# Optimization experiments

Measured on AMD Instinct MI355X. Metric: run time of the kernel, lower is better.

## Reference

```python
import jax, jax.numpy as jnp
import numpy as np

NUM_EXPERTS = 8
HIDDEN = 1024
INTER = 1024
TOKENS = 2048
TOPK = 2


def setup_inputs() -> dict:
    key = jax.random.key(0)
    ks = jax.random.split(key, 7)
    hidden_states = jax.random.normal(ks[0], (TOKENS, HIDDEN), dtype=jnp.float32)
    router_weights = jax.random.uniform(ks[1], (TOKENS, TOPK), dtype=jnp.float32)
    selected_experts = jax.random.randint(ks[2], (TOKENS, TOPK), 0, NUM_EXPERTS, dtype=jnp.int32)
    token_per_expert = jax.random.randint(ks[3], (NUM_EXPERTS,), 0, 512, dtype=jnp.int32)
    # torch Linear weight layout is [out, in]; chunked along out-dim into E experts.
    # gate/up: [E, INTER, HIDDEN]; down: [E, HIDDEN, INTER]
    scale_h = 1.0 / np.sqrt(HIDDEN)
    scale_i = 1.0 / np.sqrt(INTER)
    gate_w = jax.random.normal(ks[4], (NUM_EXPERTS, INTER, HIDDEN), dtype=jnp.float32) * scale_h
    up_w = jax.random.normal(ks[5], (NUM_EXPERTS, INTER, HIDDEN), dtype=jnp.float32) * scale_h
    down_w = jax.random.normal(ks[6], (NUM_EXPERTS, HIDDEN, INTER), dtype=jnp.float32) * scale_i
    return {
        "hidden_states": hidden_states,
        "router_weights": router_weights,
        "selected_experts": selected_experts,
        "token_per_expert": token_per_expert,
        "gate_w": gate_w,
        "up_w": up_w,
        "down_w": down_w,
    }


def reference(hidden_states, router_weights, selected_experts, token_per_expert, gate_w, up_w, down_w):
    # Math equivalent of permute -> grouped GEMM (gate/up SwiGLU, down) -> unpermute+weighted combine.
    # Each (token, k) pair is routed to expert selected_experts[t,k] and scaled by router_weights[t,k]
    # (cast to fp32 as in the original), then summed over k.
    # Grouped GEMM out = x @ W_e^T; we evaluate every expert densely over all tokens and
    # combine with a one-hot routing matrix (clean, fully vectorized reference).
    x = hidden_states  # [T, H]
    g = jnp.einsum('th,eih->eti', x, gate_w)          # [E, T, I]
    u = jnp.einsum('th,eih->eti', x, up_w)            # [E, T, I]
    h = jax.nn.silu(g) * u                            # [E, T, I]
    out_e = jnp.einsum('eti,ehi->eth', h, down_w)     # [E, T, H]
    # combine[t, e] = sum_k router_weights[t, k] * 1[selected_experts[t, k] == e]
    onehot = jax.nn.one_hot(selected_experts, NUM_EXPERTS, dtype=jnp.float32)  # [T, K, E]
    combine = jnp.einsum('tk,tke->te', router_weights.astype(jnp.float32), onehot)  # [T, E]
    y = jnp.einsum('te,eth->th', combine, out_e)      # [T, H]
    return y
```

## Files before the change

kernel.cpp:

```cpp
#include <hip/hip_runtime.h>

#define HID   1024
#define NEXP  8
#define NPAIR 4096
#define BMPAD 128
#define PERM_MAX (NPAIR + NEXP * BMPAD)
#define MT_MAX (PERM_MAX / 128)

typedef unsigned short u16;
typedef __attribute__((ext_vector_type(8))) short bf16x8;
typedef __attribute__((ext_vector_type(4))) float f32x4;
typedef __attribute__((ext_vector_type(4))) unsigned short us4;

static __device__ __forceinline__ u16 f2bf(float f) {
  union { float f; unsigned u; } v; v.f = f;
  unsigned u = v.u;
  unsigned r = (u + 0x7fffu + ((u >> 16) & 1u)) >> 16;
  return (u16)r;
}

static __device__ __forceinline__ void gload16(const void* g, void* l) {
  __builtin_amdgcn_global_load_lds(
      (const __attribute__((address_space(1))) unsigned int*)g,
      (__attribute__((address_space(3))) unsigned int*)l, 16, 0, 0);
}

static __device__ __forceinline__ f32x4 mfma_bf16(bf16x8 a, bf16x8 b, f32x4 c) {
  return __builtin_amdgcn_mfma_f32_16x16x32_bf16(a, b, c, 0, 0, 0);
}

__global__ __launch_bounds__(256) void k_prep(const float* __restrict__ x,
                                              u16* __restrict__ xb,
                                              float* __restrict__ out) {
  int i = blockIdx.x * 256 + threadIdx.x;
  int base = i * 8;
  f32x4 v0 = *(const f32x4*)(x + base);
  f32x4 v1 = *(const f32x4*)(x + base + 4);
  us4 a = { f2bf(v0[0]), f2bf(v0[1]), f2bf(v0[2]), f2bf(v0[3]) };
  us4 b = { f2bf(v1[0]), f2bf(v1[1]), f2bf(v1[2]), f2bf(v1[3]) };
  *(us4*)(xb + base)     = a;
  *(us4*)(xb + base + 4) = b;
  f32x4 z = {0.f, 0.f, 0.f, 0.f};
  *(f32x4*)(out + base)     = z;
  *(f32x4*)(out + base + 4) = z;
}

__global__ __launch_bounds__(256) void k_convw(const float* __restrict__ g,
                                               const float* __restrict__ u,
                                               const float* __restrict__ d,
                                               u16* __restrict__ gb,
                                               u16* __restrict__ ub,
                                               u16* __restrict__ db) {
  const long NTH = 3L << 20;
  for (long i = (long)blockIdx.x * 256 + threadIdx.x; i < NTH; i += (long)gridDim.x * 256) {
    int which = (int)(i >> 20);
    long off = (i & ((1L << 20) - 1)) * 8;
    const float* src = which == 0 ? g : (which == 1 ? u : d);
    u16* dst = which == 0 ? gb : (which == 1 ? ub : db);
    f32x4 v0 = *(const f32x4*)(src + off);
    f32x4 v1 = *(const f32x4*)(src + off + 4);
    us4 a = { f2bf(v0[0]), f2bf(v0[1]), f2bf(v0[2]), f2bf(v0[3]) };
    us4 b = { f2bf(v1[0]), f2bf(v1[1]), f2bf(v1[2]), f2bf(v1[3]) };
    *(us4*)(dst + off)     = a;
    *(us4*)(dst + off + 4) = b;
  }
}

__global__ __launch_bounds__(256) void k_route(const int* __restrict__ sel,
                                               int* __restrict__ hdr,
                                               int* __restrict__ perm) {
  __shared__ int cnt[NEXP];
  __shared__ int cur[NEXP];
  int tid = threadIdx.x;
  if (tid < NEXP) cnt[tid] = 0;
  __syncthreads();
  for (int p = tid; p < NPAIR; p += 256) atomicAdd(&cnt[sel[p]], 1);
  __syncthreads();
  if (tid == 0) {
    int acc = 0;
    for (int e = 0; e < NEXP; e++) {
      hdr[e] = acc;
      cur[e] = acc;
      acc += (cnt[e] + 127) & ~127;
    }
    hdr[NEXP] = acc;
  }
  __syncthreads();
  for (int i = tid; i < PERM_MAX; i += 256) perm[i] = -1;
  __syncthreads();
  for (int p = tid; p < NPAIR; p += 256) {
    int e = sel[p];
    int slot = atomicAdd(&cur[e], 1);
    perm[slot] = p;
  }
}

__global__ __launch_bounds__(256) void k_gateup(const u16* __restrict__ xb,
                                                const u16* __restrict__ gwb,
                                                const u16* __restrict__ uwb,
                                                const int* __restrict__ hdr,
                                                const int* __restrict__ perm,
                                                u16* __restrict__ hbuf) {
  __shared__ __align__(16) u16 lA[128 * 64];
  __shared__ __align__(16) u16 lBg[64 * 64];
  __shared__ __align__(16) u16 lBu[64 * 64];

  const int tid = threadIdx.x, lane = tid & 63, wv = tid >> 6;
  const int n0 = blockIdx.x * 64, m0 = blockIdx.y * 128;
  const int total = hdr[NEXP];
  if (m0 >= total) return;
  int e = 0;
  #pragma unroll
  for (int k = 1; k < NEXP; k++) if (m0 >= hdr[k]) e = k;

  const u16* srcA[4]; u16* dstA[4];
  #pragma unroll
  for (int j = 0; j < 4; j++) {
    int rt = wv * 32 + j * 8 + (lane >> 3);
    int p = perm[m0 + rt];
    int tok = (p < 0) ? 0 : (p >> 1);
    int sw = (lane & 7) ^ (rt & 7);
    srcA[j] = xb + (size_t)tok * HID + sw * 8;
    dstA[j] = &lA[(wv * 32 + j * 8) * 64];
  }
  const u16* srcG[2]; const u16* srcU[2]; int dstBo[2];
  const size_t eb = (size_t)e * (1 << 20);
  #pragma unroll
  for (int j = 0; j < 2; j++) {
    int rt = wv * 16 + j * 8 + (lane >> 3);
    int sw = (lane & 7) ^ (rt & 7);
    srcG[j] = gwb + eb + (size_t)(n0 + rt) * HID + sw * 8;
    srcU[j] = uwb + eb + (size_t)(n0 + rt) * HID + sw * 8;
    dstBo[j] = (wv * 16 + j * 8) * 64;
  }

  const int wm = wv >> 1, wn = wv & 1;
  const int fr = lane & 15, fq = lane >> 4;

  f32x4 accg[4][2], accu[4][2];
  #pragma unroll
  for (int a = 0; a < 4; a++)
    #pragma unroll
    for (int b = 0; b < 2; b++) {
      accg[a][b] = (f32x4){0.f, 0.f, 0.f, 0.f};
      accu[a][b] = (f32x4){0.f, 0.f, 0.f, 0.f};
    }

  for (int kk = 0; kk < HID / 64; kk++) {
    const int k0 = kk * 64;
    #pragma unroll
    for (int j = 0; j < 4; j++) gload16(srcA[j] + k0, dstA[j]);
    #pragma unroll
    for (int j = 0; j < 2; j++) {
      gload16(srcG[j] + k0, &lBg[dstBo[j]]);
      gload16(srcU[j] + k0, &lBu[dstBo[j]]);
    }
    __syncthreads();
    #pragma unroll
    for (int kk2 = 0; kk2 < 2; kk2++) {
      bf16x8 af[4], bg[2], bu[2];
      #pragma unroll
      for (int m2 = 0; m2 < 4; m2++) {
        int r = wm * 64 + m2 * 16 + fr, q = kk2 * 4 + fq;
        af[m2] = *(const bf16x8*)&lA[r * 64 + (q ^ (r & 7)) * 8];
      }
      #pragma unroll
      for (int n2 = 0; n2 < 2; n2++) {
        int r = wn * 32 + n2 * 16 + fr, q = kk2 * 4 + fq;
        bg[n2] = *(const bf16x8*)&lBg[r * 64 + (q ^ (r & 7)) * 8];
        bu[n2] = *(const bf16x8*)&lBu[r * 64 + (q ^ (r & 7)) * 8];
      }
      #pragma unroll
      for (int m2 = 0; m2 < 4; m2++)
        #pragma unroll
        for (int n2 = 0; n2 < 2; n2++) {
          accg[m2][n2] = mfma_bf16(af[m2], bg[n2], accg[m2][n2]);
          accu[m2][n2] = mfma_bf16(af[m2], bu[n2], accu[m2][n2]);
        }
    }
    __syncthreads();
  }

  #pragma unroll
  for (int m2 = 0; m2 < 4; m2++)
    #pragma unroll
    for (int n2 = 0; n2 < 2; n2++)
      #pragma unroll
      for (int q = 0; q < 4; q++) {
        int row = m0 + wm * 64 + m2 * 16 + fq * 4 + q;
        int col = n0 + wn * 32 + n2 * 16 + fr;
        float g = accg[m2][n2][q];
        float u = accu[m2][n2][q];
        float h = (g / (1.0f + __expf(-g))) * u;
        hbuf[(size_t)row * HID + col] = f2bf(h);
      }
}

__global__ __launch_bounds__(256) void k_down(const u16* __restrict__ hbuf,
                                              const u16* __restrict__ dwb,
                                              const int* __restrict__ hdr,
                                              const int* __restrict__ perm,
                                              const float* __restrict__ rw,
                                              float* __restrict__ out) {
  __shared__ __align__(16) u16 lA[128 * 64];
  __shared__ __align__(16) u16 lB[64 * 64];

  const int tid = threadIdx.x, lane = tid & 63, wv = tid >> 6;
  const int n0 = blockIdx.x * 64, m0 = blockIdx.y * 128;
  const int total = hdr[NEXP];
  if (m0 >= total) return;
  int e = 0;
  #pragma unroll
  for (int k = 1; k < NEXP; k++) if (m0 >= hdr[k]) e = k;

  const u16* srcA[4]; u16* dstA[4];
  #pragma unroll
  for (int j = 0; j < 4; j++) {
    int rt = wv * 32 + j * 8 + (lane >> 3);
    int sw = (lane & 7) ^ (rt & 7);
    srcA[j] = hbuf + (size_t)(m0 + rt) * HID + sw * 8;
    dstA[j] = &lA[(wv * 32 + j * 8) * 64];
  }
  const u16* srcB[2]; int dstBo[2];
  const size_t eb = (size_t)e * (1 << 20);
  #pragma unroll
  for (int j = 0; j < 2; j++) {
    int rt = wv * 16 + j * 8 + (lane >> 3);
    int sw = (lane & 7) ^ (rt & 7);
    srcB[j] = dwb + eb + (size_t)(n0 + rt) * HID + sw * 8;
    dstBo[j] = (wv * 16 + j * 8) * 64;
  }

  const int wm = wv >> 1, wn = wv & 1;
  const int fr = lane & 15, fq = lane >> 4;

  f32x4 acc[4][2];
  #pragma unroll
  for (int a = 0; a < 4; a++)
    #pragma unroll
    for (int b = 0; b < 2; b++) acc[a][b] = (f32x4){0.f, 0.f, 0.f, 0.f};

  for (int kk = 0; kk < HID / 64; kk++) {
    const int k0 = kk * 64;
    #pragma unroll
    for (int j = 0; j < 4; j++) gload16(srcA[j] + k0, dstA[j]);
    #pragma unroll
    for (int j = 0; j < 2; j++) gload16(srcB[j] + k0, &lB[dstBo[j]]);
    __syncthreads();
    #pragma unroll
    for (int kk2 = 0; kk2 < 2; kk2++) {
      bf16x8 af[4], bf[2];
      #pragma unroll
      for (int m2 = 0; m2 < 4; m2++) {
        int r = wm * 64 + m2 * 16 + fr, q = kk2 * 4 + fq;
        af[m2] = *(const bf16x8*)&lA[r * 64 + (q ^ (r & 7)) * 8];
      }
      #pragma unroll
      for (int n2 = 0; n2 < 2; n2++) {
        int r = wn * 32 + n2 * 16 + fr, q = kk2 * 4 + fq;
        bf[n2] = *(const bf16x8*)&lB[r * 64 + (q ^ (r & 7)) * 8];
      }
      #pragma unroll
      for (int m2 = 0; m2 < 4; m2++)
        #pragma unroll
        for (int n2 = 0; n2 < 2; n2++)
          acc[m2][n2] = mfma_bf16(af[m2], bf[n2], acc[m2][n2]);
    }
    __syncthreads();
  }

  #pragma unroll
  for (int m2 = 0; m2 < 4; m2++)
    #pragma unroll
    for (int q = 0; q < 4; q++) {
      int row = m0 + wm * 64 + m2 * 16 + fq * 4 + q;
      int p = perm[row];
      if (p < 0) continue;
      int t = p >> 1;
      float w = rw[p];
      #pragma unroll
      for (int n2 = 0; n2 < 2; n2++) {
        int col = n0 + wn * 32 + n2 * 16 + fr;
        atomicAdd(&out[(size_t)t * HID + col], acc[m2][n2][q] * w);
      }
    }
}

extern "C" void kernel_launch(void* const* d_in, const int* in_sizes, int n_in,
                              void* d_out, int out_size, void* d_ws, size_t ws_size,
                              hipStream_t stream) {
  const float* x   = (const float*)d_in[0];
  const float* rw  = (const float*)d_in[1];
  const int*   sel = (const int*)d_in[2];
  const float* gw  = (const float*)d_in[4];
  const float* uw  = (const float*)d_in[5];
  const float* dw  = (const float*)d_in[6];
  float* out = (float*)d_out;

  char* ws = (char*)d_ws;
  int*  hdr  = (int*)ws;
  int*  perm = (int*)(ws + 1024);
  u16*  xb   = (u16*)(ws + (1 << 16));
  u16*  gwb  = xb + (2 << 20);
  u16*  uwb  = gwb + (8 << 20);
  u16*  dwb  = uwb + (8 << 20);
  u16*  hbuf = dwb + (8 << 20);

  k_prep <<<dim3(1024), dim3(256), 0, stream>>>(x, xb, out);
  k_convw<<<dim3(4096), dim3(256), 0, stream>>>(gw, uw, dw, gwb, uwb, dwb);
  k_route<<<dim3(1),    dim3(256), 0, stream>>>(sel, hdr, perm);
  k_gateup<<<dim3(16, MT_MAX), dim3(256), 0, stream>>>(xb, gwb, uwb, hdr, perm, hbuf);
  k_down  <<<dim3(16, MT_MAX), dim3(256), 0, stream>>>(hbuf, dwb, hdr, perm, rw, out);
}
```

Before: 114.4 us.

## Pre-permute activations and remap GEMM grids to expert-major tile loops

Weight conversion and output zeroing are merged into one fixed-grid kernel, and activations are gathered and converted into a permuted bf16 buffer by a new kernel. The GEMM kernels no longer do an indirect per-row gather. Both GEMM kernels now use a 1D grid indexed by expert, N tile and M-tile slot, with each block looping over that expert's M tiles at a stride of 8. This drops the blocks that exited early and keeps the same expert's weights hot across consecutive tiles. The cost is an extra pass writing and reading the permuted activation buffer, and possible imbalance when one expert has many more M tiles than others.

Result: slower. 133.9 us (+17.1%).

```diff
diff --git a/kernel.cpp b/kernel.cpp
--- a/kernel.cpp
+++ b/kernel.cpp
@@ -1,11 +1,11 @@
 #include <hip/hip_runtime.h>
+#include <hip/hip_bf16.h>
 
 #define HID   1024
 #define NEXP  8
 #define NPAIR 4096
-#define BMPAD 128
-#define PERM_MAX (NPAIR + NEXP * BMPAD)
-#define MT_MAX (PERM_MAX / 128)
+#define PERM_MAX (NPAIR + NEXP * 128)
+#define MT_CAP 8
 
 typedef unsigned short u16;
 typedef __attribute__((ext_vector_type(8))) short bf16x8;
@@ -19,6 +19,15 @@
   return (u16)r;
 }
 
+static __device__ __forceinline__ void conv8(const float* src, u16* dst) {
+  f32x4 v0 = *(const f32x4*)src;
+  f32x4 v1 = *(const f32x4*)(src + 4);
+  us4 a = { f2bf(v0[0]), f2bf(v0[1]), f2bf(v0[2]), f2bf(v0[3]) };
+  us4 b = { f2bf(v1[0]), f2bf(v1[1]), f2bf(v1[2]), f2bf(v1[3]) };
+  *(us4*)dst       = a;
+  *(us4*)(dst + 4) = b;
+}
+
 static __device__ __forceinline__ void gload16(const void* g, void* l) {
   __builtin_amdgcn_global_load_lds(
       (const __attribute__((address_space(1))) unsigned int*)g,
@@ -27,43 +36,6 @@
 
 static __device__ __forceinline__ f32x4 mfma_bf16(bf16x8 a, bf16x8 b, f32x4 c) {
   return __builtin_amdgcn_mfma_f32_16x16x32_bf16(a, b, c, 0, 0, 0);
-}
-
-__global__ __launch_bounds__(256) void k_prep(const float* __restrict__ x,
-                                              u16* __restrict__ xb,
-                                              float* __restrict__ out) {
-  int i = blockIdx.x * 256 + threadIdx.x;
-  int base = i * 8;
-  f32x4 v0 = *(const f32x4*)(x + base);
-  f32x4 v1 = *(const f32x4*)(x + base + 4);
-  us4 a = { f2bf(v0[0]), f2bf(v0[1]), f2bf(v0[2]), f2bf(v0[3]) };
-  us4 b = { f2bf(v1[0]), f2bf(v1[1]), f2bf(v1[2]), f2bf(v1[3]) };
-  *(us4*)(xb + base)     = a;
-  *(us4*)(xb + base + 4) = b;
-  f32x4 z = {0.f, 0.f, 0.f, 0.f};
-  *(f32x4*)(out + base)     = z;
-  *(f32x4*)(out + base + 4) = z;
-}
-
-__global__ __launch_bounds__(256) void k_convw(const float* __restrict__ g,
-                                               const float* __restrict__ u,
-                                               const float* __restrict__ d,
-                                               u16* __restrict__ gb,
-                                               u16* __restrict__ ub,
-                                               u16* __restrict__ db) {
-  const long NTH = 3L << 20;
-  for (long i = (long)blockIdx.x * 256 + threadIdx.x; i < NTH; i += (long)gridDim.x * 256) {
-    int which = (int)(i >> 20);
-    long off = (i & ((1L << 20) - 1)) * 8;
-    const float* src = which == 0 ? g : (which == 1 ? u : d);
-    u16* dst = which == 0 ? gb : (which == 1 ? ub : db);
-    f32x4 v0 = *(const f32x4*)(src + off);
-    f32x4 v1 = *(const f32x4*)(src + off + 4);
-    us4 a = { f2bf(v0[0]), f2bf(v0[1]), f2bf(v0[2]), f2bf(v0[3]) };
-    us4 b = { f2bf(v1[0]), f2bf(v1[1]), f2bf(v1[2]), f2bf(v1[3]) };
-    *(us4*)(dst + off)     = a;
-    *(us4*)(dst + off + 4) = b;
-  }
 }
 
 __global__ __launch_bounds__(256) void k_route(const int* __restrict__ sel,
@@ -95,36 +67,61 @@
   }
 }
 
-__global__ __launch_bounds__(256) void k_gateup(const u16* __restrict__ xb,
+__global__ __launch_bounds__(256) void k_conv(const float* __restrict__ g,
+                                              const float* __restrict__ u,
+                                              const float* __restrict__ d,
+                                              u16* __restrict__ gb,
+                                              u16* __restrict__ ub,
+                                              u16* __restrict__ db,
+                                              float* __restrict__ out) {
+  const int i = blockIdx.x * 256 + threadIdx.x;
+  #pragma unroll
+  for (int j = 0; j < 6; j++) {
+    long c = (long)i + 524288L * j;
+    int which = (int)(c >> 20);
+    long off = (c & ((1L << 20) - 1)) * 8;
+    const float* src = which == 0 ? g : (which == 1 ? u : d);
+    u16* dst = which == 0 ? gb : (which == 1 ? ub : db);
+    conv8(src + off, dst + off);
+  }
+  f32x4 z = {0.f, 0.f, 0.f, 0.f};
+  *(f32x4*)(out + (long)i * 4) = z;
+}
+
+__global__ __launch_bounds__(256) void k_perm(const float* __restrict__ x,
+                                              const int* __restrict__ perm,
+                                              u16* __restrict__ xp) {
+  int c = blockIdx.x * 256 + threadIdx.x;
+  int r = c >> 7, kq = c & 127;
+  int p = perm[r];
+  int tok = (p < 0) ? 0 : (p >> 1);
+  conv8(x + (size_t)tok * HID + kq * 8, xp + (size_t)r * HID + kq * 8);
+}
+
+__global__ __launch_bounds__(256) void k_gateup(const u16* __restrict__ xp,
                                                 const u16* __restrict__ gwb,
                                                 const u16* __restrict__ uwb,
                                                 const int* __restrict__ hdr,
-                                                const int* __restrict__ perm,
                                                 u16* __restrict__ hbuf) {
   __shared__ __align__(16) u16 lA[128 * 64];
   __shared__ __align__(16) u16 lBg[64 * 64];
   __shared__ __align__(16) u16 lBu[64 * 64];
 
   const int tid = threadIdx.x, lane = tid & 63, wv = tid >> 6;
-  const int n0 = blockIdx.x * 64, m0 = blockIdx.y * 128;
-  const int total = hdr[NEXP];
-  if (m0 >= total) return;
-  int e = 0;
-  #pragma unroll
-  for (int k = 1; k < NEXP; k++) if (m0 >= hdr[k]) e = k;
-
-  const u16* srcA[4]; u16* dstA[4];
-  #pragma unroll
-  for (int j = 0; j < 4; j++) {
-    int rt = wv * 32 + j * 8 + (lane >> 3);
-    int p = perm[m0 + rt];
-    int tok = (p < 0) ? 0 : (p >> 1);
-    int sw = (lane & 7) ^ (rt & 7);
-    srcA[j] = xb + (size_t)tok * HID + sw * 8;
-    dstA[j] = &lA[(wv * 32 + j * 8) * 64];
-  }
+  const int bid = blockIdx.x;
+  const int e = bid & 7;
+  const int idx = bid >> 3;
+  const int mt0 = idx & 7;
+  const int nt = idx >> 3;
+  const int seg0 = hdr[e];
+  const int mcnt = (hdr[e + 1] - seg0) >> 7;
+  const int n0 = nt * 64;
+
+  const int wm = wv >> 1, wn = wv & 1;
+  const int fr = lane & 15, fq = lane >> 4;
+  const size_t eb = (size_t)e << 20;
+
   const u16* srcG[2]; const u16* srcU[2]; int dstBo[2];
-  const size_t eb = (size_t)e * (1 << 20);
   #pragma unroll
   for (int j = 0; j < 2; j++) {
     int rt = wv * 16 + j * 8 + (lane >> 3);
@@ -134,66 +131,75 @@
     dstBo[j] = (wv * 16 + j * 8) * 64;
   }
 
-  const int wm = wv >> 1, wn = wv & 1;
-  const int fr = lane & 15, fq = lane >> 4;
-
-  f32x4 accg[4][2], accu[4][2];
-  #pragma unroll
-  for (int a = 0; a < 4; a++)
-    #pragma unroll
-    for (int b = 0; b < 2; b++) {
-      accg[a][b] = (f32x4){0.f, 0.f, 0.f, 0.f};
-      accu[a][b] = (f32x4){0.f, 0.f, 0.f, 0.f};
-    }
-
-  for (int kk = 0; kk < HID / 64; kk++) {
-    const int k0 = kk * 64;
-    #pragma unroll
-    for (int j = 0; j < 4; j++) gload16(srcA[j] + k0, dstA[j]);
-    #pragma unroll
-    for (int j = 0; j < 2; j++) {
-      gload16(srcG[j] + k0, &lBg[dstBo[j]]);
-      gload16(srcU[j] + k0, &lBu[dstBo[j]]);
-    }
-    __syncthreads();
-    #pragma unroll
-    for (int kk2 = 0; kk2 < 2; kk2++) {
-      bf16x8 af[4], bg[2], bu[2];
-      #pragma unroll
-      for (int m2 = 0; m2 < 4; m2++) {
-        int r = wm * 64 + m2 * 16 + fr, q = kk2 * 4 + fq;
-        af[m2] = *(const bf16x8*)&lA[r * 64 + (q ^ (r & 7)) * 8];
-      }
-      #pragma unroll
-      for (int n2 = 0; n2 < 2; n2++) {
-        int r = wn * 32 + n2 * 16 + fr, q = kk2 * 4 + fq;
-        bg[n2] = *(const bf16x8*)&lBg[r * 64 + (q ^ (r & 7)) * 8];
-        bu[n2] = *(const bf16x8*)&lBu[r * 64 + (q ^ (r & 7)) * 8];
-      }
-      #pragma unroll
-      for (int m2 = 0; m2 < 4; m2++)
+  for (int mt = mt0; mt < mcnt; mt += MT_CAP) {
+    const int m0 = seg0 + mt * 128;
+    const u16* srcA[4]; int dstAo[4];
+    #pragma unroll
+    for (int j = 0; j < 4; j++) {
+      int rt = wv * 32 + j * 8 + (lane >> 3);
+      int sw = (lane & 7) ^ (rt & 7);
+      srcA[j] = xp + (size_t)(m0 + rt) * HID + sw * 8;
+      dstAo[j] = (wv * 32 + j * 8) * 64;
+    }
+
+    f32x4 accg[4][2], accu[4][2];
+    #pragma unroll
+    for (int a = 0; a < 4; a++)
+      #pragma unroll
+      for (int b = 0; b < 2; b++) {
+        accg[a][b] = (f32x4){0.f, 0.f, 0.f, 0.f};
+        accu[a][b] = (f32x4){0.f, 0.f, 0.f, 0.f};
+      }
+
+    for (int kk = 0; kk < 16; kk++) {
+      const int k0 = kk * 64;
+      #pragma unroll
+      for (int j = 0; j < 4; j++) gload16(srcA[j] + k0, &lA[dstAo[j]]);
+      #pragma unroll
+      for (int j = 0; j < 2; j++) {
+        gload16(srcG[j] + k0, &lBg[dstBo[j]]);
+        gload16(srcU[j] + k0, &lBu[dstBo[j]]);
+      }
+      __syncthreads();
+      #pragma unroll
+      for (int kk2 = 0; kk2 < 2; kk2++) {
+        bf16x8 af[4], bg[2], bu[2];
+        #pragma unroll
+        for (int m2 = 0; m2 < 4; m2++) {
+          int r = wm * 64 + m2 * 16 + fr, q = kk2 * 4 + fq;
+          af[m2] = *(const bf16x8*)&lA[r * 64 + (q ^ (r & 7)) * 8];
+        }
         #pragma unroll
         for (int n2 = 0; n2 < 2; n2++) {
-          accg[m2][n2] = mfma_bf16(af[m2], bg[n2], accg[m2][n2]);
-          accu[m2][n2] = mfma_bf16(af[m2], bu[n2], accu[m2][n2]);
-        }
-    }
-    __syncthreads();
-  }
-
-  #pragma unroll
-  for (int m2 = 0; m2 < 4; m2++)
-    #pragma unroll
-    for (int n2 = 0; n2 < 2; n2++)
-      #pragma unroll
-      for (int q = 0; q < 4; q++) {
-        int row = m0 + wm * 64 + m2 * 16 + fq * 4 + q;
-        int col = n0 + wn * 32 + n2 * 16 + fr;
-        float g = accg[m2][n2][q];
-        float u = accu[m2][n2][q];
-        float h = (g / (1.0f + __expf(-g))) * u;
-        hbuf[(size_t)row * HID + col] = f2bf(h);
-      }
+          int r = wn * 32 + n2 * 16 + fr, q = kk2 * 4 + fq;
+          bg[n2] = *(const bf16x8*)&lBg[r * 64 + (q ^ (r & 7)) * 8];
+          bu[n2] = *(const bf16x8*)&lBu[r * 64 + (q ^ (r & 7)) * 8];
+        }
+        #pragma unroll
+        for (int m2 = 0; m2 < 4; m2++)
+          #pragma unroll
+          for (int n2 = 0; n2 < 2; n2++) {
+            accg[m2][n2] = mfma_bf16(af[m2], bg[n2], accg[m2][n2]);
+            accu[m2][n2] = mfma_bf16(af[m2], bu[n2], accu[m2][n2]);
+          }
+      }
+      __syncthreads();
+    }
+
+    #pragma unroll
+    for (int m2 = 0; m2 < 4; m2++)
+      #pragma unroll
+      for (int n2 = 0; n2 < 2; n2++)
+        #pragma unroll
+        for (int q = 0; q < 4; q++) {
+          int row = m0 + wm * 64 + m2 * 16 + fq * 4 + q;
+          int col = n0 + wn * 32 + n2 * 16 + fr;
+          float g = accg[m2][n2][q];
+          float u = accu[m2][n2][q];
+          float h = (g / (1.0f + __expf(-g))) * u;
+          hbuf[(size_t)row * HID + col] = f2bf(h);
+        }
+  }
 }
 
 __global__ __launch_bounds__(256) void k_down(const u16* __restrict__ hbuf,
@@ -206,23 +212,20 @@
   __shared__ __align__(16) u16 lB[64 * 64];
 
   const int tid = threadIdx.x, lane = tid & 63, wv = tid >> 6;
-  const int n0 = blockIdx.x * 64, m0 = blockIdx.y * 128;
-  const int total = hdr[NEXP];
-  if (m0 >= total) return;
-  int e = 0;
-  #pragma unroll
-  for (int k = 1; k < NEXP; k++) if (m0 >= hdr[k]) e = k;
-
-  const u16* srcA[4]; u16* dstA[4];
-  #pragma unroll
-  for (int j = 0; j < 4; j++) {
-    int rt = wv * 32 + j * 8 + (lane >> 3);
-    int sw = (lane & 7) ^ (rt & 7);
-    srcA[j] = hbuf + (size_t)(m0 + rt) * HID + sw * 8;
-    dstA[j] = &lA[(wv * 32 + j * 8) * 64];
-  }
+  const int bid = blockIdx.x;
+  const int e = bid & 7;
+  const int idx = bid >> 3;
+  const int mt0 = idx & 7;
+  const int nt = idx >> 3;
+  const int seg0 = hdr[e];
+  const int mcnt = (hdr[e + 1] - seg0) >> 7;
+  const int n0 = nt * 64;
+
+  const int wm = wv >> 1, wn = wv & 1;
+  const int fr = lane & 15, fq = lane >> 4;
+  const size_t eb = (size_t)e << 20;
+
   const u16* srcB[2]; int dstBo[2];
-  const size_t eb = (size_t)e * (1 << 20);
   #pragma unroll
   for (int j = 0; j < 2; j++) {
     int rt = wv * 16 + j * 8 + (lane >> 3);
@@ -231,59 +234,68 @@
     dstBo[j] = (wv * 16 + j * 8) * 64;
   }
 
-  const int wm = wv >> 1, wn = wv & 1;
-  const int fr = lane & 15, fq = lane >> 4;
-
-  f32x4 acc[4][2];
-  #pragma unroll
-  for (int a = 0; a < 4; a++)
-    #pragma unroll
-    for (int b = 0; b < 2; b++) acc[a][b] = (f32x4){0.f, 0.f, 0.f, 0.f};
-
-  for (int kk = 0; kk < HID / 64; kk++) {
-    const int k0 = kk * 64;
-    #pragma unroll
-    for (int j = 0; j < 4; j++) gload16(srcA[j] + k0, dstA[j]);
-    #pragma unroll
-    for (int j = 0; j < 2; j++) gload16(srcB[j] + k0, &lB[dstBo[j]]);
-    __syncthreads();
-    #pragma unroll
-    for (int kk2 = 0; kk2 < 2; kk2++) {
-      bf16x8 af[4], bf[2];
-      #pragma unroll
-      for (int m2 = 0; m2 < 4; m2++) {
-        int r = wm * 64 + m2 * 16 + fr, q = kk2 * 4 + fq;
-        af[m2] = *(const bf16x8*)&lA[r * 64 + (q ^ (r & 7)) * 8];
-      }
-      #pragma unroll
-      for (int n2 = 0; n2 < 2; n2++) {
-        int r = wn * 32 + n2 * 16 + fr, q = kk2 * 4 + fq;
-        bf[n2] = *(const bf16x8*)&lB[r * 64 + (q ^ (r & 7)) * 8];
-      }
-      #pragma unroll
-      for (int m2 = 0; m2 < 4; m2++)
-        #pragma unroll
-        for (int n2 = 0; n2 < 2; n2++)
-          acc[m2][n2] = mfma_bf16(af[m2], bf[n2], acc[m2][n2]);
-    }
-    __syncthreads();
-  }
-
-  #pragma unroll
-  for (int m2 = 0; m2 < 4; m2++)
-    #pragma unroll
-    for (int q = 0; q < 4; q++) {
-      int row = m0 + wm * 64 + m2 * 16 + fq * 4 + q;
-      int p = perm[row];
-      if (p < 0) continue;
-      int t = p >> 1;
-      float w = rw[p];
-      #pragma unroll
-      for (int n2 = 0; n2 < 2; n2++) {
-        int col = n0 + wn * 32 + n2 * 16 + fr;
-        atomicAdd(&out[(size_t)t * HID + col], acc[m2][n2][q] * w);
-      }
-    }
+  for (int mt = mt0; mt < mcnt; mt += MT_CAP) {
+    const int m0 = seg0 + mt * 128;
+    const u16* srcA[4]; int dstAo[4];
+    #pragma unroll
+    for (int j = 0; j < 4; j++) {
+      int rt = wv * 32 + j * 8 + (lane >> 3);
+      int sw = (lane & 7) ^ (rt & 7);
+      srcA[j] = hbuf + (size_t)(m0 + rt) * HID + sw * 8;
+      dstAo[j] = (wv * 32 + j * 8) * 64;
+    }
+
+    f32x4 acc[4][2];
+    #pragma unroll
+    for (int a = 0; a < 4; a++)
+      #pragma unroll
+      for (int b = 0; b < 2; b++) acc[a][b] = (f32x4){0.f, 0.f, 0.f, 0.f};
+
+    for (int kk = 0; kk < 16; kk++) {
+      const int k0 = kk * 64;
+      #pragma unroll
+      for (int j = 0; j < 4; j++) gload16(srcA[j] + k0, &lA[dstAo[j]]);
+      #pragma unroll
+      for (int j = 0; j < 2; j++) gload16(srcB[j] + k0, &lB[dstBo[j]]);
+      __syncthreads();
+      #pragma unroll
+      for (int kk2 = 0; kk2 < 2; kk2++) {
+        bf16x8 af[4], bf[2];
+        #pragma unroll
+        for (int m2 = 0; m2 < 4; m2++) {
+          int r = wm * 64 + m2 * 16 + fr, q = kk2 * 4 + fq;
+          af[m2] = *(const bf16x8*)&lA[r * 64 + (q ^ (r & 7)) * 8];
+        }
+        #pragma unroll
+        for (int n2 = 0; n2 < 2; n2++) {
+          int r = wn * 32 + n2 * 16 + fr, q = kk2 * 4 + fq;
+          bf[n2] = *(const bf16x8*)&lB[r * 64 + (q ^ (r & 7)) * 8];
+        }
+        #pragma unroll
+        for (int m2 = 0; m2 < 4; m2++)
+          #pragma unroll
+          for (int n2 = 0; n2 < 2; n2++)
+            acc[m2][n2] = mfma_bf16(af[m2], bf[n2], acc[m2][n2]);
+      }
+      __syncthreads();
+    }
+
+    #pragma unroll
+    for (int m2 = 0; m2 < 4; m2++)
+      #pragma unroll
+      for (int q = 0; q < 4; q++) {
+        int row = m0 + wm * 64 + m2 * 16 + fq * 4 + q;
+        int p = perm[row];
+        if (p < 0) continue;
+        int t = p >> 1;
+        float w = rw[p];
+        #pragma unroll
+        for (int n2 = 0; n2 < 2; n2++) {
+          int col = n0 + wn * 32 + n2 * 16 + fr;
+          atomicAdd(&out[(size_t)t * HID + col], acc[m2][n2][q] * w);
+        }
+      }
+  }
 }
 
 extern "C" void kernel_launch(void* const* d_in, const int* in_sizes, int n_in,
@@ -300,15 +312,15 @@
   char* ws = (char*)d_ws;
   int*  hdr  = (int*)ws;
   int*  perm = (int*)(ws + 1024);
-  u16*  xb   = (u16*)(ws + (1 << 16));
-  u16*  gwb  = xb + (2 << 20);
+  u16*  xp   = (u16*)(ws + (1 << 16));
+  u16*  gwb  = xp + (PERM_MAX * HID);
   u16*  uwb  = gwb + (8 << 20);
   u16*  dwb  = uwb + (8 << 20);
   u16*  hbuf = dwb + (8 << 20);
 
-  k_prep <<<dim3(1024), dim3(256), 0, stream>>>(x, xb, out);
-  k_convw<<<dim3(4096), dim3(256), 0, stream>>>(gw, uw, dw, gwb, uwb, dwb);
-  k_route<<<dim3(1),    dim3(256), 0, stream>>>(sel, hdr, perm);
-  k_gateup<<<dim3(16, MT_MAX), dim3(256), 0, stream>>>(xb, gwb, uwb, hdr, perm, hbuf);
-  k_down  <<<dim3(16, MT_MAX), dim3(256), 0, stream>>>(hbuf, dwb, hdr, perm, rw, out);
-}
+  k_route <<<dim3(1),    dim3(256), 0, stream>>>(sel, hdr, perm);
+  k_conv  <<<dim3(2048), dim3(256), 0, stream>>>(gw, uw, dw, gwb, uwb, dwb, out);
+  k_perm  <<<dim3(2560), dim3(256), 0, stream>>>(x, perm, xp);
+  k_gateup<<<dim3(8 * 16 * MT_CAP), dim3(256), 0, stream>>>(xp, gwb, uwb, hdr, hbuf);
+  k_down  <<<dim3(8 * 16 * MT_CAP), dim3(256), 0, stream>>>(hbuf, dwb, hdr, perm, rw, out);
+}
```
